# Kernel tuning notes

Hardware: AMD Instinct MI355X
Metric: run time of the kernel (lower is better)

Reference implementation:

```python
import jax, jax.numpy as jnp
import numpy as np

N_EMBD = 1024
H_DIM = 1024
NB = 16          # blocks resolved by _find_dynamic_num_blocks for all projections
N_MEM = 128
N_FORG = H_DIM - N_MEM
RANK = 64
LOG_DT_INIT = -2.0
EPS = 1.1920929e-07  # torch fp32 finfo eps used by F.rms_norm


def rms_norm(x):
    return x * jax.lax.rsqrt(jnp.mean(jnp.square(x), axis=-1, keepdims=True) + EPS)


def silu(x):
    return x * jax.nn.sigmoid(x)


def blockdiag(x, w):
    # x: [..., nb*bi], w: [nb, bo, bi] -> [..., nb*bo]
    nb, bo, bi = w.shape
    xs = x.reshape(*x.shape[:-1], nb, bi)
    y = jnp.einsum('...ni,noi->...no', xs, w)
    return y.reshape(*x.shape[:-1], nb * bo)


def causal_scan(drive, a):
    # drive: [B,T,D] float32, a: [D] per-channel decay; causal conv with kernel a^t via FFT
    B, T, D = drive.shape
    steps = jnp.arange(T, dtype=jnp.float32)
    kernel = jnp.exp(jnp.log(jnp.maximum(a, 1e-6))[:, None] * steps[None, :])  # [D,T]
    n_fft = 1 << int(2 * T - 1).bit_length()
    df = jnp.fft.rfft(drive.astype(jnp.float32).transpose(0, 2, 1), n=n_fft, axis=-1)
    kf = jnp.fft.rfft(kernel, n=n_fft, axis=-1)
    y = jnp.fft.irfft(df * kf[None], n=n_fft, axis=-1)[..., :T]
    return y.transpose(0, 2, 1).astype(drive.dtype)


def geom_gain(a, K):
    one_minus = 1.0 - a
    safe = jnp.maximum(one_minus, 1e-8)
    return jnp.where(jnp.abs(one_minus) < 1e-6,
                     jnp.full_like(a, float(K)),
                     (1.0 - a ** K) / safe)


def setup_inputs() -> dict:
    key = jax.random.key(0)
    ks = jax.random.split(key, 10)
    s = 0.02
    bi_e, bo_h = N_EMBD // NB, H_DIM // NB
    bi_p = (2 * N_EMBD + H_DIM) // NB
    bo_e = N_EMBD // NB
    return {
        'x': jax.random.normal(ks[0], (4, 4096, N_EMBD), dtype=jnp.float32),
        'active_k': 4,
        'b_seq_w': jax.random.normal(ks[1], (NB, bo_h, bi_e), jnp.float32) * s,
        'b_depth_w': jax.random.normal(ks[2], (NB, bo_h, bi_e), jnp.float32) * s,
        'w_post_w': jax.random.normal(ks[3], (NB, bo_h, bi_p), jnp.float32) * s,
        'w_local_w': jax.random.normal(ks[4], (NB, bo_e, H_DIM // NB), jnp.float32) * s,
        'lr_A': jax.random.normal(ks[5], (N_EMBD, RANK), jnp.float32) * s,
        'lr_B': jax.random.normal(ks[6], (RANK, H_DIM), jnp.float32) * s,
        'log_A_seq': jnp.zeros((H_DIM,), jnp.float32),
        'log_dt_seq': jnp.full((H_DIM,), LOG_DT_INIT, jnp.float32),
        'log_A_depth': jnp.zeros((N_FORG,), jnp.float32),
        'log_dt_depth': jnp.full((N_FORG,), LOG_DT_INIT, jnp.float32),
    }


def reference(x, active_k, b_seq_w, b_depth_w, w_post_w, w_local_w, lr_A, lr_B,
              log_A_seq, log_dt_seq, log_A_depth, log_dt_depth):
    K = int(active_k)
    e = rms_norm(x)
    shifted_e = jnp.pad(e[:, :-1], ((0, 0), (1, 0), (0, 0)))
    a_seq = jnp.exp(-jnp.exp(log_A_seq) * jnp.exp(log_dt_seq))
    h_seq = causal_scan(silu(blockdiag(e, b_seq_w)), a_seq)
    a_forg = jnp.exp(-jnp.exp(log_A_depth) * jnp.exp(log_dt_depth))
    a_depth = jnp.concatenate([jnp.ones((N_MEM,), a_forg.dtype), a_forg], axis=0)
    gain = geom_gain(a_depth, K).astype(x.dtype)
    h_depth = gain * silu(blockdiag(e, b_depth_w))
    h = h_seq + h_depth
    r = silu(blockdiag(jnp.concatenate([rms_norm(h), e, shifted_e], axis=-1), w_post_w))
    out = x + blockdiag(r, w_local_w) + (r @ lr_B.T) @ lr_A.T
    return out
```

## Files before the change

kernel.cpp:

```cpp
#include <hip/hip_runtime.h>

#define B_ 4
#define T_ 4096
#define D_ 1024
#define R_ (B_*T_)
#define CHUNK_ 64
#define NCH_ (T_/CHUNK_)
#define EPS_ 1.1920929e-07f

typedef unsigned short ushort_t;
typedef __attribute__((ext_vector_type(8))) short short8;
typedef __attribute__((ext_vector_type(4))) float f32x4;

__device__ __forceinline__ float silu_f(float v){ return v / (1.0f + __expf(-v)); }

__device__ __forceinline__ ushort_t f2bf(float f){
    unsigned u = __float_as_uint(f);
    unsigned r = u + 0x7fffu + ((u>>16)&1u);
    return (ushort_t)(r>>16);
}
__device__ __forceinline__ float bf2f(ushort_t s){ return __uint_as_float(((unsigned)s)<<16); }

__device__ __forceinline__ f32x4 mfma16(short8 a, short8 b, f32x4 c){
    return __builtin_amdgcn_mfma_f32_16x16x32_bf16(a, b, c, 0, 0, 0);
}

__global__ void prep_k(const float* __restrict__ s0, const float* __restrict__ s1,
                       const float* __restrict__ s2, const float* __restrict__ s3,
                       const float* __restrict__ s4, const float* __restrict__ s5,
                       ushort_t* __restrict__ d0, ushort_t* __restrict__ d1,
                       ushort_t* __restrict__ d2, ushort_t* __restrict__ d3,
                       ushort_t* __restrict__ d4, ushort_t* __restrict__ d5,
                       const float* __restrict__ logA_seq, const float* __restrict__ logdt_seq,
                       const float* __restrict__ logA_dep, const float* __restrict__ logdt_dep,
                       const int* __restrict__ active_k,
                       float* __restrict__ aseq, float* __restrict__ apowC, float* __restrict__ gain){
    int i = blockIdx.x*256 + threadIdx.x;
    if      (i < 65536)   d0[i] = f2bf(s0[i]);
    else if (i < 131072)  d1[i-65536] = f2bf(s1[i-65536]);
    else if (i < 327680)  d2[i-131072] = f2bf(s2[i-131072]);
    else if (i < 393216)  d3[i-327680] = f2bf(s3[i-327680]);
    else if (i < 458752)  d4[i-393216] = f2bf(s4[i-393216]);
    else if (i < 524288)  d5[i-458752] = f2bf(s5[i-458752]);
    else if (i < 524288 + D_){
        int d = i - 524288;
        float K = (float)(*active_k);
        float a = expf(-expf(logA_seq[d]) * expf(logdt_seq[d]));
        a = fmaxf(a, 1e-6f);
        aseq[d] = a;
        apowC[d] = powf(a, (float)CHUNK_);
        float g;
        if (d < 128) {
            g = K;
        } else {
            float ad = expf(-expf(logA_dep[d-128]) * expf(logdt_dep[d-128]));
            float om = 1.0f - ad;
            if (fabsf(om) < 1e-6f) g = K;
            else g = (1.0f - powf(ad, K)) / fmaxf(om, 1e-8f);
        }
        gain[d] = g;
    }
}

__global__ __launch_bounds__(256) void rmsbf_k(const float* __restrict__ x, ushort_t* __restrict__ e){
    int row = blockIdx.x;
    int tid = threadIdx.x;
    float4 v = ((const float4*)(x + (size_t)row*D_))[tid];
    float ss = v.x*v.x + v.y*v.y + v.z*v.z + v.w*v.w;
    for (int off=32; off; off>>=1) ss += __shfl_down(ss, off, 64);
    __shared__ float red[4];
    if ((tid&63)==0) red[tid>>6] = ss;
    __syncthreads();
    float tot = red[0]+red[1]+red[2]+red[3];
    float scale = 1.0f / sqrtf(tot*(1.0f/D_) + EPS_);
    ushort4 o;
    o.x = f2bf(v.x*scale); o.y = f2bf(v.y*scale); o.z = f2bf(v.z*scale); o.w = f2bf(v.w*scale);
    ((ushort4*)(e + (size_t)row*D_))[tid] = o;
}

__global__ __launch_bounds__(256) void bd2s_k(const ushort_t* __restrict__ e,
        const ushort_t* __restrict__ wseq, const ushort_t* __restrict__ wdep,
        const float* __restrict__ gain, const float* __restrict__ aseq,
        ushort_t* __restrict__ hsum, float* __restrict__ carry){
    __shared__ __align__(16) ushort_t sd[4][16][72];
    __shared__ __align__(16) ushort_t sh[4][16][72];
    int wave = threadIdx.x>>6, lane = threadIdx.x&63;
    int m = lane&15, quad = lane>>4;
    int orow = lane>>2, oq = lane&3;
    int n = blockIdx.y;
    int chunk0 = blockIdx.x*256 + wave*64;

    short8 bs[2][4], bd[2][4];
    #pragma unroll
    for (int s=0;s<2;++s)
        #pragma unroll
        for (int c=0;c<4;++c){
            bs[s][c] = *(const short8*)(wseq + n*4096 + (c*16+m)*64 + s*32 + quad*8);
            bd[s][c] = *(const short8*)(wdep + n*4096 + (c*16+m)*64 + s*32 + quad*8);
        }
    float g[4];
    #pragma unroll
    for (int c=0;c<4;++c) g[c] = gain[n*64 + c*16 + m];

    float a = aseq[n*64 + lane];
    float hh = 0.f;

    #pragma unroll
    for (int t=0;t<4;++t){
        int r0 = chunk0 + t*16;
        const ushort_t* ab = e + (size_t)(r0+m)*D_ + n*64 + quad*8;
        short8 a0 = *(const short8*)ab;
        short8 a1 = *(const short8*)(ab + 32);
        f32x4 accs[4], accd[4];
        #pragma unroll
        for (int c=0;c<4;++c){
            accs[c]=(f32x4)0.f; accd[c]=(f32x4)0.f;
            accs[c]=mfma16(a0, bs[0][c], accs[c]);
            accd[c]=mfma16(a0, bd[0][c], accd[c]);
            accs[c]=mfma16(a1, bs[1][c], accs[c]);
            accd[c]=mfma16(a1, bd[1][c], accd[c]);
        }
        #pragma unroll
        for (int c=0;c<4;++c)
            #pragma unroll
            for (int r=0;r<4;++r){
                sd[wave][quad*4+r][c*16+m] = f2bf(silu_f(accs[c][r]));
                sh[wave][quad*4+r][c*16+m] = f2bf(g[c]*silu_f(accd[c][r]));
            }
        #pragma unroll
        for (int s=0;s<16;++s){
            hh = fmaf(a, hh, bf2f(sd[wave][s][lane]));
            sd[wave][s][lane] = f2bf(hh + bf2f(sh[wave][s][lane]));
        }
        ushort_t* db = hsum + (size_t)(r0+orow)*D_ + n*64;
        #pragma unroll
        for (int it=0;it<2;++it)
            *(short8*)(db + (it*4+oq)*8) = *(const short8*)&sd[wave][orow][(it*4+oq)*8];
    }
    carry[(size_t)(chunk0>>6)*D_ + n*64 + lane] = hh;
}

__global__ __launch_bounds__(256) void scan2_k(float* __restrict__ carry, const float* __restrict__ apowC){
    int tid = blockIdx.x*256 + threadIdx.x;
    int d = tid & (D_-1);
    int b = tid >> 10;
    float aC = apowC[d];
    float pref = 0.f;
    for (int c=0;c<NCH_;++c){
        size_t idx = (size_t)(b*NCH_+c)*D_ + d;
        float s = carry[idx];
        carry[idx] = pref;
        pref = fmaf(aC, pref, s);
    }
}

__global__ __launch_bounds__(256) void scan3_k(const ushort_t* __restrict__ hsum,
                                               const float* __restrict__ aseq,
                                               const float* __restrict__ carry,
                                               ushort_t* __restrict__ h){
    int tid = blockIdx.x*256 + threadIdx.x;
    int d  = tid & (D_-1);
    int bc = tid >> 10;
    int c  = bc & (NCH_-1);
    int b  = bc >> 6;
    float a = aseq[d];
    float P = carry[(size_t)bc*D_ + d];
    size_t base = ((size_t)(b*T_ + c*CHUNK_))*D_ + d;
    float apow = a;
    #pragma unroll 4
    for (int s=0; s<CHUNK_; ++s){
        size_t idx = base + (size_t)s*D_;
        h[idx] = f2bf(bf2f(hsum[idx]) + P*apow);
        apow *= a;
    }
}

__global__ __launch_bounds__(256) void scale_k(const ushort_t* __restrict__ h, float* __restrict__ scale){
    int wave = threadIdx.x>>6, lane = threadIdx.x&63;
    int row = blockIdx.x*4 + wave;
    const ushort_t* hb = h + (size_t)row*D_ + lane*16;
    short8 v0 = *(const short8*)hb;
    short8 v1 = *(const short8*)(hb + 8);
    float ss = 0.f;
    #pragma unroll
    for (int j=0;j<8;++j){ float f0 = bf2f((ushort_t)v0[j]); float f1 = bf2f((ushort_t)v1[j]); ss += f0*f0 + f1*f1; }
    for (int off=32; off; off>>=1) ss += __shfl_down(ss, off, 64);
    if (lane==0) scale[row] = rsqrtf(ss*(1.0f/D_) + EPS_);
}

__global__ __launch_bounds__(256) void post_k(const ushort_t* __restrict__ h,
                                              const float* __restrict__ scale,
                                              const ushort_t* __restrict__ e,
                                              const ushort_t* __restrict__ wpost, ushort_t* __restrict__ rout){
    __shared__ __align__(16) ushort_t st[4][16][72];
    int wave = threadIdx.x>>6, lane = threadIdx.x&63;
    int m = lane&15, quad = lane>>4;
    int orow = lane>>2, oq = lane&3;
    int n = blockIdx.y;
    int row0 = blockIdx.x*128 + wave*32 + m;

    float scl[2];
    #pragma unroll
    for (int t=0;t<2;++t) scl[t] = (n*192 < 1024) ? scale[row0 + t*16] : 0.f;

    f32x4 acc[2][4];
    #pragma unroll
    for (int t=0;t<2;++t)
        #pragma unroll
        for (int c=0;c<4;++c) acc[t][c]=(f32x4)0.f;

    #pragma unroll 1
    for (int s=0;s<6;++s){
        int g0 = n*192 + s*32;
        short8 bw[4];
        #pragma unroll
        for (int c=0;c<4;++c)
            bw[c] = *(const short8*)(wpost + n*(64*192) + (c*16+m)*192 + s*32 + quad*8);
        #pragma unroll
        for (int t=0;t<2;++t){
            int row = row0 + t*16;
            short8 af;
            if (g0 < 1024){
                short8 hv = *(const short8*)(h + (size_t)row*D_ + g0 + quad*8);
                float sc = scl[t];
                #pragma unroll
                for (int j=0;j<8;++j) af[j] = (short)f2bf(bf2f((ushort_t)hv[j])*sc);
            } else if (g0 < 2048){
                af = *(const short8*)(e + (size_t)row*D_ + (g0-1024) + quad*8);
            } else {
                if ((row & (T_-1)) == 0) af = short8{0,0,0,0,0,0,0,0};
                else af = *(const short8*)(e + (size_t)(row-1)*D_ + (g0-2048) + quad*8);
            }
            #pragma unroll
            for (int c=0;c<4;++c)
                acc[t][c] = mfma16(af, bw[c], acc[t][c]);
        }
    }
    #pragma unroll
    for (int t=0;t<2;++t){
        int r0 = blockIdx.x*128 + wave*32 + t*16;
        #pragma unroll
        for (int c=0;c<4;++c)
            #pragma unroll
            for (int r=0;r<4;++r)
                st[wave][quad*4+r][c*16+m] = f2bf(silu_f(acc[t][c][r]));
        ushort_t* db = rout + (size_t)(r0+orow)*D_ + n*64;
        #pragma unroll
        for (int it=0;it<2;++it)
            *(short8*)(db + (it*4+oq)*8) = *(const short8*)&st[wave][orow][(it*4+oq)*8];
    }
}

__global__ __launch_bounds__(256) void rlow_k(const ushort_t* __restrict__ r, const ushort_t* __restrict__ lrB,
                                              ushort_t* __restrict__ rlow){
    __shared__ __align__(16) float sacc[4][16][68];
    int wave = threadIdx.x>>6, lane = threadIdx.x&63;
    int m = lane&15, quad = lane>>4;
    int r0 = blockIdx.x*16;
    f32x4 acc[4];
    #pragma unroll
    for (int c=0;c<4;++c) acc[c]=(f32x4)0.f;
    const ushort_t* ab = r + (size_t)(r0+m)*D_ + wave*256 + quad*8;
    #pragma unroll
    for (int s=0;s<8;++s){
        short8 a = *(const short8*)(ab + s*32);
        #pragma unroll
        for (int c=0;c<4;++c){
            short8 b = *(const short8*)(lrB + (c*16+m)*1024 + wave*256 + s*32 + quad*8);
            acc[c] = mfma16(a, b, acc[c]);
        }
    }
    #pragma unroll
    for (int c=0;c<4;++c)
        #pragma unroll
        for (int r2=0;r2<4;++r2)
            sacc[wave][quad*4+r2][c*16+m] = acc[c][r2];
    __syncthreads();
    int row  = threadIdx.x>>4;
    int col4 = (threadIdx.x&15)*4;
    float4 v0 = *(const float4*)&sacc[0][row][col4];
    float4 v1 = *(const float4*)&sacc[1][row][col4];
    float4 v2 = *(const float4*)&sacc[2][row][col4];
    float4 v3 = *(const float4*)&sacc[3][row][col4];
    ushort4 o;
    o.x = f2bf(v0.x+v1.x+v2.x+v3.x);
    o.y = f2bf(v0.y+v1.y+v2.y+v3.y);
    o.z = f2bf(v0.z+v1.z+v2.z+v3.z);
    o.w = f2bf(v0.w+v1.w+v2.w+v3.w);
    *(ushort4*)(rlow + (size_t)(r0+row)*64 + col4) = o;
}

__global__ __launch_bounds__(256) void out_k(const float* __restrict__ x, const ushort_t* __restrict__ r,
        const ushort_t* __restrict__ rlow, const ushort_t* __restrict__ wloc, const ushort_t* __restrict__ lrA,
        float* __restrict__ out){
    __shared__ __align__(16) float st[4][16][68];
    int wave = threadIdx.x>>6, lane = threadIdx.x&63;
    int m = lane&15, quad = lane>>4;
    int orow = lane>>2, oq = lane&3;
    int n = blockIdx.y;

    short8 wl[2][4], la[4][2];
    #pragma unroll
    for (int c=0;c<4;++c)
        #pragma unroll
        for (int s=0;s<2;++s){
            wl[s][c] = *(const short8*)(wloc + n*4096 + (c*16+m)*64 + s*32 + quad*8);
            la[c][s] = *(const short8*)(lrA + (size_t)(n*64 + c*16 + m)*64 + s*32 + quad*8);
        }
    #pragma unroll
    for (int t=0;t<2;++t){
        int r0 = blockIdx.x*128 + wave*32 + t*16;
        const float* xb = x + (size_t)(r0+orow)*D_ + n*64;
        float4 xv[4];
        #pragma unroll
        for (int it=0;it<4;++it) xv[it] = *(const float4*)(xb + (it*4+oq)*4);

        const ushort_t* lb = rlow + (size_t)(r0+m)*64 + quad*8;
        short8 al0 = *(const short8*)lb;
        short8 al1 = *(const short8*)(lb + 32);
        const ushort_t* ab = r + (size_t)(r0+m)*D_ + n*64 + quad*8;
        short8 ar0 = *(const short8*)ab;
        short8 ar1 = *(const short8*)(ab + 32);
        f32x4 acc[4];
        #pragma unroll
        for (int c=0;c<4;++c){
            acc[c]=(f32x4)0.f;
            acc[c]=mfma16(al0, la[c][0], acc[c]);
            acc[c]=mfma16(al1, la[c][1], acc[c]);
            acc[c]=mfma16(ar0, wl[0][c], acc[c]);
            acc[c]=mfma16(ar1, wl[1][c], acc[c]);
        }
        #pragma unroll
        for (int c=0;c<4;++c)
            #pragma unroll
            for (int r2=0;r2<4;++r2)
                st[wave][quad*4+r2][c*16+m] = acc[c][r2];
        float* ob = out + (size_t)(r0+orow)*D_ + n*64;
        #pragma unroll
        for (int it=0;it<4;++it){
            float4 v = *(const float4*)&st[wave][orow][(it*4+oq)*4];
            v.x += xv[it].x; v.y += xv[it].y; v.z += xv[it].z; v.w += xv[it].w;
            *(float4*)(ob + (it*4+oq)*4) = v;
        }
    }
}

extern "C" void kernel_launch(void* const* d_in, const int* in_sizes, int n_in,
                              void* d_out, int out_size, void* d_ws, size_t ws_size,
                              hipStream_t stream) {
    const float* x         = (const float*)d_in[0];
    const int*   active_k  = (const int*)  d_in[1];
    const float* b_seq_w   = (const float*)d_in[2];
    const float* b_depth_w = (const float*)d_in[3];
    const float* w_post_w  = (const float*)d_in[4];
    const float* w_local_w = (const float*)d_in[5];
    const float* lr_A      = (const float*)d_in[6];
    const float* lr_B      = (const float*)d_in[7];
    const float* logA_seq  = (const float*)d_in[8];
    const float* logdt_seq = (const float*)d_in[9];
    const float* logA_dep  = (const float*)d_in[10];
    const float* logdt_dep = (const float*)d_in[11];

    float* ws    = (float*)d_ws;
    float* carry = ws;
    float* aseq  = carry + (size_t)B_*NCH_*D_;
    float* apowC = aseq + D_;
    float* gain  = apowC + D_;
    float* scale = gain + D_;
    ushort_t* ub       = (ushort_t*)(scale + R_);
    ushort_t* e_bf     = ub;
    ushort_t* hsum_bf  = e_bf + (size_t)R_*D_;
    ushort_t* h_bf     = hsum_bf + (size_t)R_*D_;
    ushort_t* r_bf     = h_bf + (size_t)R_*D_;
    ushort_t* rlow_bf  = r_bf + (size_t)R_*D_;
    ushort_t* wseq_bf  = rlow_bf + (size_t)R_*64;
    ushort_t* wdep_bf  = wseq_bf + 65536;
    ushort_t* wpost_bf = wdep_bf + 65536;
    ushort_t* wloc_bf  = wpost_bf + 196608;
    ushort_t* lrA_bf   = wloc_bf + 65536;
    ushort_t* lrB_bf   = lrA_bf + 65536;

    prep_k<<<(524288 + D_ + 255)/256, 256, 0, stream>>>(
        b_seq_w, b_depth_w, w_post_w, w_local_w, lr_A, lr_B,
        wseq_bf, wdep_bf, wpost_bf, wloc_bf, lrA_bf, lrB_bf,
        logA_seq, logdt_seq, logA_dep, logdt_dep, active_k, aseq, apowC, gain);

    rmsbf_k<<<R_, 256, 0, stream>>>(x, e_bf);
    bd2s_k <<<dim3(R_/256, 16), 256, 0, stream>>>(e_bf, wseq_bf, wdep_bf, gain, aseq,
                                                  hsum_bf, carry);
    scan2_k<<<(B_*D_)/256, 256, 0, stream>>>(carry, apowC);
    scan3_k<<<(B_*NCH_*D_)/256, 256, 0, stream>>>(hsum_bf, aseq, carry, h_bf);
    scale_k<<<R_/4, 256, 0, stream>>>(h_bf, scale);
    post_k <<<dim3(R_/128, 16), 256, 0, stream>>>(h_bf, scale, e_bf, wpost_bf, r_bf);
    rlow_k <<<R_/16, 256, 0, stream>>>(r_bf, lrB_bf, rlow_bf);
    out_k  <<<dim3(R_/128, 16), 256, 0, stream>>>(x, r_bf, rlow_bf, wloc_bf, lrA_bf, (float*)d_out);
}
```

Measured before the change: 285.8 us.

## Store bf16 activations in panel-major layout and vectorize scan3

Intermediate bf16 tensors (e, hsum, h, r) move from row-major [R,1024] to 16 panels of [R,64], so each 64-column block is contiguous across rows. All producers and consumers are updated to index the panels, and scan3 now processes 8 channels per thread with 16-byte loads and stores. The goal is denser, more coalesced accesses in the per-block GEMM kernels and the scan. The cost is more scattered accesses where kernels span all columns of a row (scale_k, rlow_k, the rmsnorm store).

```diff
diff --git a/kernel.cpp b/kernel.cpp
--- a/kernel.cpp
+++ b/kernel.cpp
@@ -7,6 +7,7 @@
 #define CHUNK_ 64
 #define NCH_ (T_/CHUNK_)
 #define EPS_ 1.1920929e-07f
+#define P_ ((size_t)R_*64)
 
 typedef unsigned short ushort_t;
 typedef __attribute__((ext_vector_type(8))) short short8;
@@ -24,6 +25,7 @@
 __device__ __forceinline__ f32x4 mfma16(short8 a, short8 b, f32x4 c){
     return __builtin_amdgcn_mfma_f32_16x16x32_bf16(a, b, c, 0, 0, 0);
 }
+
 
 __global__ void prep_k(const float* __restrict__ s0, const float* __restrict__ s1,
                        const float* __restrict__ s2, const float* __restrict__ s3,
@@ -75,7 +77,8 @@
     float scale = 1.0f / sqrtf(tot*(1.0f/D_) + EPS_);
     ushort4 o;
     o.x = f2bf(v.x*scale); o.y = f2bf(v.y*scale); o.z = f2bf(v.z*scale); o.w = f2bf(v.w*scale);
-    ((ushort4*)(e + (size_t)row*D_))[tid] = o;
+    int col = tid*4;
+    *(ushort4*)(e + (size_t)(col>>6)*P_ + (size_t)row*64 + (col&63)) = o;
 }
 
 __global__ __launch_bounds__(256) void bd2s_k(const ushort_t* __restrict__ e,
@@ -108,7 +111,7 @@
     #pragma unroll
     for (int t=0;t<4;++t){
         int r0 = chunk0 + t*16;
-        const ushort_t* ab = e + (size_t)(r0+m)*D_ + n*64 + quad*8;
+        const ushort_t* ab = e + (size_t)n*P_ + (size_t)(r0+m)*64 + quad*8;
         short8 a0 = *(const short8*)ab;
         short8 a1 = *(const short8*)(ab + 32);
         f32x4 accs[4], accd[4];
@@ -132,7 +135,7 @@
             hh = fmaf(a, hh, bf2f(sd[wave][s][lane]));
             sd[wave][s][lane] = f2bf(hh + bf2f(sh[wave][s][lane]));
         }
-        ushort_t* db = hsum + (size_t)(r0+orow)*D_ + n*64;
+        ushort_t* db = hsum + (size_t)n*P_ + (size_t)(r0+orow)*64;
         #pragma unroll
         for (int it=0;it<2;++it)
             *(short8*)(db + (it*4+oq)*8) = *(const short8*)&sd[wave][orow][(it*4+oq)*8];
@@ -159,26 +162,38 @@
                                                const float* __restrict__ carry,
                                                ushort_t* __restrict__ h){
     int tid = blockIdx.x*256 + threadIdx.x;
-    int d  = tid & (D_-1);
-    int bc = tid >> 10;
+    int d0g  = (tid&7)*8;
+    int trip = tid>>3;
+    int n  = trip & 15;
+    int bc = trip >> 4;
+    int b  = bc >> 6;
     int c  = bc & (NCH_-1);
-    int b  = bc >> 6;
-    float a = aseq[d];
-    float P = carry[(size_t)bc*D_ + d];
-    size_t base = ((size_t)(b*T_ + c*CHUNK_))*D_ + d;
-    float apow = a;
-    #pragma unroll 4
+    int d  = n*64 + d0g;
+    float a[8], P[8], apow[8];
+    #pragma unroll
+    for (int j=0;j<8;++j){
+        a[j] = aseq[d+j];
+        P[j] = carry[(size_t)bc*D_ + d + j];
+        apow[j] = a[j];
+    }
+    size_t base = (size_t)n*P_ + (size_t)(b*T_ + c*CHUNK_)*64 + d0g;
     for (int s=0; s<CHUNK_; ++s){
-        size_t idx = base + (size_t)s*D_;
-        h[idx] = f2bf(bf2f(hsum[idx]) + P*apow);
-        apow *= a;
+        short8 v = *(const short8*)(hsum + base + (size_t)s*64);
+        short8 o;
+        #pragma unroll
+        for (int j=0;j<8;++j){
+            o[j] = (short)f2bf(bf2f((ushort_t)v[j]) + P[j]*apow[j]);
+            apow[j] *= a[j];
+        }
+        *(short8*)(h + base + (size_t)s*64) = o;
     }
 }
 
 __global__ __launch_bounds__(256) void scale_k(const ushort_t* __restrict__ h, float* __restrict__ scale){
     int wave = threadIdx.x>>6, lane = threadIdx.x&63;
     int row = blockIdx.x*4 + wave;
-    const ushort_t* hb = h + (size_t)row*D_ + lane*16;
+    int pl = lane>>2, q = lane&3;
+    const ushort_t* hb = h + (size_t)pl*P_ + (size_t)row*64 + q*16;
     short8 v0 = *(const short8*)hb;
     short8 v1 = *(const short8*)(hb + 8);
     float ss = 0.f;
@@ -221,15 +236,17 @@
             int row = row0 + t*16;
             short8 af;
             if (g0 < 1024){
-                short8 hv = *(const short8*)(h + (size_t)row*D_ + g0 + quad*8);
+                short8 hv = *(const short8*)(h + (size_t)(g0>>6)*P_ + (size_t)row*64 + (g0&63) + quad*8);
                 float sc = scl[t];
                 #pragma unroll
                 for (int j=0;j<8;++j) af[j] = (short)f2bf(bf2f((ushort_t)hv[j])*sc);
             } else if (g0 < 2048){
-                af = *(const short8*)(e + (size_t)row*D_ + (g0-1024) + quad*8);
+                int ge = g0 - 1024;
+                af = *(const short8*)(e + (size_t)(ge>>6)*P_ + (size_t)row*64 + (ge&63) + quad*8);
             } else {
+                int ge = g0 - 2048;
                 if ((row & (T_-1)) == 0) af = short8{0,0,0,0,0,0,0,0};
-                else af = *(const short8*)(e + (size_t)(row-1)*D_ + (g0-2048) + quad*8);
+                else af = *(const short8*)(e + (size_t)(ge>>6)*P_ + (size_t)(row-1)*64 + (ge&63) + quad*8);
             }
             #pragma unroll
             for (int c=0;c<4;++c)
@@ -244,7 +261,7 @@
             #pragma unroll
             for (int r=0;r<4;++r)
                 st[wave][quad*4+r][c*16+m] = f2bf(silu_f(acc[t][c][r]));
-        ushort_t* db = rout + (size_t)(r0+orow)*D_ + n*64;
+        ushort_t* db = rout + (size_t)n*P_ + (size_t)(r0+orow)*64;
         #pragma unroll
         for (int it=0;it<2;++it)
             *(short8*)(db + (it*4+oq)*8) = *(const short8*)&st[wave][orow][(it*4+oq)*8];
@@ -260,13 +277,13 @@
     f32x4 acc[4];
     #pragma unroll
     for (int c=0;c<4;++c) acc[c]=(f32x4)0.f;
-    const ushort_t* ab = r + (size_t)(r0+m)*D_ + wave*256 + quad*8;
     #pragma unroll
     for (int s=0;s<8;++s){
-        short8 a = *(const short8*)(ab + s*32);
+        int col = wave*256 + s*32;
+        short8 a = *(const short8*)(r + (size_t)(col>>6)*P_ + (size_t)(r0+m)*64 + (col&63) + quad*8);
         #pragma unroll
         for (int c=0;c<4;++c){
-            short8 b = *(const short8*)(lrB + (c*16+m)*1024 + wave*256 + s*32 + quad*8);
+            short8 b = *(const short8*)(lrB + (c*16+m)*1024 + col + quad*8);
             acc[c] = mfma16(a, b, acc[c]);
         }
     }
@@ -318,7 +335,7 @@
         const ushort_t* lb = rlow + (size_t)(r0+m)*64 + quad*8;
         short8 al0 = *(const short8*)lb;
         short8 al1 = *(const short8*)(lb + 32);
-        const ushort_t* ab = r + (size_t)(r0+m)*D_ + n*64 + quad*8;
+        const ushort_t* ab = r + (size_t)n*P_ + (size_t)(r0+m)*64 + quad*8;
         short8 ar0 = *(const short8*)ab;
         short8 ar1 = *(const short8*)(ab + 32);
         f32x4 acc[4];
@@ -389,7 +406,7 @@
     bd2s_k <<<dim3(R_/256, 16), 256, 0, stream>>>(e_bf, wseq_bf, wdep_bf, gain, aseq,
                                                   hsum_bf, carry);
     scan2_k<<<(B_*D_)/256, 256, 0, stream>>>(carry, apowC);
-    scan3_k<<<(B_*NCH_*D_)/256, 256, 0, stream>>>(hsum_bf, aseq, carry, h_bf);
+    scan3_k<<<(B_*NCH_*D_/8)/256, 256, 0, stream>>>(hsum_bf, aseq, carry, h_bf);
     scale_k<<<R_/4, 256, 0, stream>>>(h_bf, scale);
     post_k <<<dim3(R_/128, 16), 256, 0, stream>>>(h_bf, scale, e_bf, wpost_bf, r_bf);
     rlow_k <<<R_/16, 256, 0, stream>>>(r_bf, lrB_bf, rlow_bf);
```

After: 292.6 us. 1.02x slower.

## Fuse scan fixup with RMS-norm scaling and store pre-normalized h

Applied to the files above, without the earlier changes.

The per-chunk scan correction, the row RMS-norm reduction and the bf16 scaling are merged into one kernel. It handles 8 rows per block with vectorized 8-channel loads and reads decay powers from a table built in the prep kernel. The post GEMM then reads already-normalized h directly, which removes the separate scale kernel, a full extra read of h, and the per-element rescaling inside the GEMM loop. The cost is a 64xD power table, per-row shuffle reductions plus block syncs in the scan kernel, and a serial 64-step loop per channel added to prep.

```diff
diff --git a/kernel.cpp b/kernel.cpp
--- a/kernel.cpp
+++ b/kernel.cpp
@@ -34,7 +34,8 @@
                        const float* __restrict__ logA_seq, const float* __restrict__ logdt_seq,
                        const float* __restrict__ logA_dep, const float* __restrict__ logdt_dep,
                        const int* __restrict__ active_k,
-                       float* __restrict__ aseq, float* __restrict__ apowC, float* __restrict__ gain){
+                       float* __restrict__ aseq, float* __restrict__ apowC,
+                       float* __restrict__ gain, float* __restrict__ apowtab){
     int i = blockIdx.x*256 + threadIdx.x;
     if      (i < 65536)   d0[i] = f2bf(s0[i]);
     else if (i < 131072)  d1[i-65536] = f2bf(s1[i-65536]);
@@ -49,6 +50,8 @@
         a = fmaxf(a, 1e-6f);
         aseq[d] = a;
         apowC[d] = powf(a, (float)CHUNK_);
+        float ap = a;
+        for (int s2=0;s2<CHUNK_;++s2){ apowtab[s2*D_ + d] = ap; ap *= a; }
         float g;
         if (d < 128) {
             g = K;
@@ -154,42 +157,67 @@
     }
 }
 
-__global__ __launch_bounds__(256) void scan3_k(const ushort_t* __restrict__ hsum,
-                                               const float* __restrict__ aseq,
-                                               const float* __restrict__ carry,
-                                               ushort_t* __restrict__ h){
-    int tid = blockIdx.x*256 + threadIdx.x;
-    int d  = tid & (D_-1);
-    int bc = tid >> 10;
-    int c  = bc & (NCH_-1);
-    int b  = bc >> 6;
-    float a = aseq[d];
-    float P = carry[(size_t)bc*D_ + d];
-    size_t base = ((size_t)(b*T_ + c*CHUNK_))*D_ + d;
-    float apow = a;
-    #pragma unroll 4
-    for (int s=0; s<CHUNK_; ++s){
-        size_t idx = base + (size_t)s*D_;
-        h[idx] = f2bf(bf2f(hsum[idx]) + P*apow);
-        apow *= a;
-    }
-}
-
-__global__ __launch_bounds__(256) void scale_k(const ushort_t* __restrict__ h, float* __restrict__ scale){
-    int wave = threadIdx.x>>6, lane = threadIdx.x&63;
-    int row = blockIdx.x*4 + wave;
-    const ushort_t* hb = h + (size_t)row*D_ + lane*16;
-    short8 v0 = *(const short8*)hb;
-    short8 v1 = *(const short8*)(hb + 8);
-    float ss = 0.f;
-    #pragma unroll
-    for (int j=0;j<8;++j){ float f0 = bf2f((ushort_t)v0[j]); float f1 = bf2f((ushort_t)v1[j]); ss += f0*f0 + f1*f1; }
-    for (int off=32; off; off>>=1) ss += __shfl_down(ss, off, 64);
-    if (lane==0) scale[row] = rsqrtf(ss*(1.0f/D_) + EPS_);
-}
-
-__global__ __launch_bounds__(256) void post_k(const ushort_t* __restrict__ h,
-                                              const float* __restrict__ scale,
+__global__ __launch_bounds__(256) void scan3s_k(const ushort_t* __restrict__ hsum,
+                                                const float* __restrict__ aseq,
+                                                const float* __restrict__ carry,
+                                                const float* __restrict__ apowtab,
+                                                ushort_t* __restrict__ hn){
+    __shared__ float part[4][4];
+    __shared__ float scl[8];
+    int tid = threadIdx.x;
+    int lane = tid & 63, wave = tid >> 6;
+    int cg = tid & 127;
+    int rp = tid >> 7;
+    int d0 = cg*8;
+    int row0 = blockIdx.x*8;
+    int bc = row0 >> 6;
+    int s0 = row0 & 63;
+
+    float a2[8], P[8], apow[8];
+    #pragma unroll
+    for (int j=0;j<8;++j){
+        float aj = aseq[d0+j];
+        a2[j] = aj*aj;
+        P[j]  = carry[(size_t)bc*D_ + d0 + j];
+        apow[j] = apowtab[(size_t)(s0 + rp)*D_ + d0 + j];
+    }
+
+    float hf[4][8];
+    #pragma unroll
+    for (int i=0;i<4;++i){
+        int row = row0 + i*2 + rp;
+        short8 v = *(const short8*)(hsum + (size_t)row*D_ + d0);
+        float ss = 0.f;
+        #pragma unroll
+        for (int j=0;j<8;++j){
+            float f = bf2f((ushort_t)v[j]) + P[j]*apow[j];
+            hf[i][j] = f;
+            ss += f*f;
+            apow[j] *= a2[j];
+        }
+        for (int off=32; off; off>>=1) ss += __shfl_down(ss, off, 64);
+        if (lane==0) part[wave][i] = ss;
+    }
+    __syncthreads();
+    if (tid < 8){
+        int r = tid;
+        int rr = r & 1, ii = r >> 1;
+        float sum = part[rr*2][ii] + part[rr*2+1][ii];
+        scl[r] = rsqrtf(sum*(1.0f/D_) + EPS_);
+    }
+    __syncthreads();
+    #pragma unroll
+    for (int i=0;i<4;++i){
+        int rloc = i*2 + rp;
+        float sc = scl[rloc];
+        short8 o;
+        #pragma unroll
+        for (int j=0;j<8;++j) o[j] = (short)f2bf(hf[i][j]*sc);
+        *(short8*)(hn + (size_t)(row0 + rloc)*D_ + d0) = o;
+    }
+}
+
+__global__ __launch_bounds__(256) void post_k(const ushort_t* __restrict__ hn,
                                               const ushort_t* __restrict__ e,
                                               const ushort_t* __restrict__ wpost, ushort_t* __restrict__ rout){
     __shared__ __align__(16) ushort_t st[4][16][72];
@@ -199,10 +227,6 @@
     int n = blockIdx.y;
     int row0 = blockIdx.x*128 + wave*32 + m;
 
-    float scl[2];
-    #pragma unroll
-    for (int t=0;t<2;++t) scl[t] = (n*192 < 1024) ? scale[row0 + t*16] : 0.f;
-
     f32x4 acc[2][4];
     #pragma unroll
     for (int t=0;t<2;++t)
@@ -221,10 +245,7 @@
             int row = row0 + t*16;
             short8 af;
             if (g0 < 1024){
-                short8 hv = *(const short8*)(h + (size_t)row*D_ + g0 + quad*8);
-                float sc = scl[t];
-                #pragma unroll
-                for (int j=0;j<8;++j) af[j] = (short)f2bf(bf2f((ushort_t)hv[j])*sc);
+                af = *(const short8*)(hn + (size_t)row*D_ + g0 + quad*8);
             } else if (g0 < 2048){
                 af = *(const short8*)(e + (size_t)row*D_ + (g0-1024) + quad*8);
             } else {
@@ -361,17 +382,17 @@
     const float* logA_dep  = (const float*)d_in[10];
     const float* logdt_dep = (const float*)d_in[11];
 
-    float* ws    = (float*)d_ws;
-    float* carry = ws;
-    float* aseq  = carry + (size_t)B_*NCH_*D_;
-    float* apowC = aseq + D_;
-    float* gain  = apowC + D_;
-    float* scale = gain + D_;
-    ushort_t* ub       = (ushort_t*)(scale + R_);
+    float* ws      = (float*)d_ws;
+    float* carry   = ws;
+    float* aseq    = carry + (size_t)B_*NCH_*D_;
+    float* apowC   = aseq + D_;
+    float* gain    = apowC + D_;
+    float* apowtab = gain + D_;
+    ushort_t* ub       = (ushort_t*)(apowtab + (size_t)CHUNK_*D_);
     ushort_t* e_bf     = ub;
     ushort_t* hsum_bf  = e_bf + (size_t)R_*D_;
-    ushort_t* h_bf     = hsum_bf + (size_t)R_*D_;
-    ushort_t* r_bf     = h_bf + (size_t)R_*D_;
+    ushort_t* hn_bf    = hsum_bf + (size_t)R_*D_;
+    ushort_t* r_bf     = hn_bf + (size_t)R_*D_;
     ushort_t* rlow_bf  = r_bf + (size_t)R_*D_;
     ushort_t* wseq_bf  = rlow_bf + (size_t)R_*64;
     ushort_t* wdep_bf  = wseq_bf + 65536;
@@ -383,15 +404,14 @@
     prep_k<<<(524288 + D_ + 255)/256, 256, 0, stream>>>(
         b_seq_w, b_depth_w, w_post_w, w_local_w, lr_A, lr_B,
         wseq_bf, wdep_bf, wpost_bf, wloc_bf, lrA_bf, lrB_bf,
-        logA_seq, logdt_seq, logA_dep, logdt_dep, active_k, aseq, apowC, gain);
-
-    rmsbf_k<<<R_, 256, 0, stream>>>(x, e_bf);
-    bd2s_k <<<dim3(R_/256, 16), 256, 0, stream>>>(e_bf, wseq_bf, wdep_bf, gain, aseq,
-                                                  hsum_bf, carry);
-    scan2_k<<<(B_*D_)/256, 256, 0, stream>>>(carry, apowC);
-    scan3_k<<<(B_*NCH_*D_)/256, 256, 0, stream>>>(hsum_bf, aseq, carry, h_bf);
-    scale_k<<<R_/4, 256, 0, stream>>>(h_bf, scale);
-    post_k <<<dim3(R_/128, 16), 256, 0, stream>>>(h_bf, scale, e_bf, wpost_bf, r_bf);
-    rlow_k <<<R_/16, 256, 0, stream>>>(r_bf, lrB_bf, rlow_bf);
-    out_k  <<<dim3(R_/128, 16), 256, 0, stream>>>(x, r_bf, rlow_bf, wloc_bf, lrA_bf, (float*)d_out);
-}
+        logA_seq, logdt_seq, logA_dep, logdt_dep, active_k, aseq, apowC, gain, apowtab);
+
+    rmsbf_k <<<R_, 256, 0, stream>>>(x, e_bf);
+    bd2s_k  <<<dim3(R_/256, 16), 256, 0, stream>>>(e_bf, wseq_bf, wdep_bf, gain, aseq,
+                                                   hsum_bf, carry);
+    scan2_k <<<(B_*D_)/256, 256, 0, stream>>>(carry, apowC);
+    scan3s_k<<<R_/8, 256, 0, stream>>>(hsum_bf, aseq, carry, apowtab, hn_bf);
+    post_k  <<<dim3(R_/128, 16), 256, 0, stream>>>(hn_bf, e_bf, wpost_bf, r_bf);
+    rlow_k  <<<R_/16, 256, 0, stream>>>(r_bf, lrB_bf, rlow_bf);
+    out_k   <<<dim3(R_/128, 16), 256, 0, stream>>>(x, r_bf, rlow_bf, wloc_bf, lrA_bf, (float*)d_out);
+}
```

Result: faster. 271.6 us (-5.0%).
